# Kernel tuning notes

Measured on AMD Instinct MI355X. Metric: run time of the kernel, lower is better.

Reference implementation:

```python
import jax, jax.numpy as jnp
import numpy as np

N1, N2 = 262144, 65536          # dense / coarse point counts (packed batch)
PREV, SKIP, M0, M1 = 512, 256, 256, 256
EPS_BN = 1e-5                    # torch BatchNorm1d default eps
EPS_DIST = 1e-8


def _bn(x, g, b):
    # BatchNorm1d in training mode: biased batch stats over the point axis
    m = x.mean(axis=0)
    v = x.var(axis=0)
    return (x - m) * jax.lax.rsqrt(v + EPS_BN) * g + b


def setup_inputs() -> dict:
    key = jax.random.key(0)
    ks = jax.random.split(key, 8)
    inp = {
        "points1": jax.random.normal(ks[0], (N1, SKIP), jnp.float32),
        "points2": jax.random.normal(ks[1], (N2, PREV), jnp.float32),
        "dist": jax.random.uniform(ks[2], (N1, 3), jnp.float32),
        "idx": jax.random.randint(ks[3], (N1, 3), 0, N2, dtype=jnp.int32),
        # mlp_f0 / norm_f0
        "Wf0": jax.random.normal(ks[4], (PREV, M0), jnp.float32) / np.sqrt(PREV).astype(np.float32),
        "bf0": jnp.zeros((M0,), jnp.float32),
        "gf0": jnp.ones((M0,), jnp.float32),
        "betaf0": jnp.zeros((M0,), jnp.float32),
        # mlp_s0 / norm_s0 (skip path)
        "Ws0": jax.random.normal(ks[5], (SKIP, M0), jnp.float32) / np.sqrt(SKIP).astype(np.float32),
        "bs0": jnp.zeros((M0,), jnp.float32),
        "gs0": jnp.ones((M0,), jnp.float32),
        "betas0": jnp.zeros((M0,), jnp.float32),
        # mlp_convs[0] / mlp_bns[0]
        "W1": jax.random.normal(ks[6], (M0, M1), jnp.float32) / np.sqrt(M0).astype(np.float32),
        "b1": jnp.zeros((M1,), jnp.float32),
        "g1": jnp.ones((M1,), jnp.float32),
        "beta1": jnp.zeros((M1,), jnp.float32),
    }
    return inp


def reference(points1, points2, dist, idx, Wf0, bf0, gf0, betaf0,
              Ws0, bs0, gs0, betas0, W1, b1, g1, beta1):
    # f0 MLP + BN on coarse features: [N2, PREV] -> [N2, M0]
    p2 = _bn(points2 @ Wf0 + bf0, gf0, betaf0)
    # inverse-distance weights over 3 neighbors: [N1, 3]
    dr = 1.0 / (dist + EPS_DIST)
    w = dr / dr.sum(axis=1, keepdims=True)
    # fused gather + weighted sum: p2[idx] is [N1, 3, M0]
    interp = jnp.einsum('nkc,nk->nc', p2[idx], w)
    # skip path: [N1, SKIP] -> [N1, M0]
    skip = _bn(points1 @ Ws0 + bs0, gs0, betas0)
    x = jax.nn.relu(interp + skip)
    # mlp_convs stack (one layer here): Linear + BN + ReLU
    x = jax.nn.relu(_bn(x @ W1 + b1, g1, beta1))
    return x
```

## Files before the change

kernel.cpp:

```cpp
#include <hip/hip_runtime.h>
#include <hip/hip_bf16.h>

#define CN1 262144
#define CN2 65536
#define CPREV 512
#define CSKIP 256

using u16 = unsigned short;

typedef __attribute__((ext_vector_type(8))) short short8;
typedef __attribute__((ext_vector_type(8))) unsigned short ushort8;
typedef __attribute__((ext_vector_type(4))) float f32x4;
typedef __attribute__((ext_vector_type(8))) float f32x8;

__device__ __forceinline__ float toF(float v) { return v; }
__device__ __forceinline__ float toF(u16 u) { return __uint_as_float(((unsigned)u) << 16); }
__device__ __forceinline__ u16 f2bf(float f) {
    unsigned b = __float_as_uint(f);
    b += 0x7FFFu + ((b >> 16) & 1u);
    return (u16)(b >> 16);
}
__device__ __forceinline__ unsigned pack2(float lo, float hi) {
    return ((unsigned)f2bf(hi) << 16) | (unsigned)f2bf(lo);
}

__global__ __launch_bounds__(256) void transpose_all(
    const float* __restrict__ Wf0, const float* __restrict__ Ws0,
    const float* __restrict__ W1,
    u16* __restrict__ Wtf0, u16* __restrict__ Wts0, u16* __restrict__ Wt1)
{
    int b = blockIdx.x;
    const float* W; u16* Wt; int ksh, e;
    if (b < 512)      { W = Wf0; Wt = Wtf0; ksh = 9; e = b * 256 + threadIdx.x; }
    else if (b < 768) { W = Ws0; Wt = Wts0; ksh = 8; e = (b - 512) * 256 + threadIdx.x; }
    else              { W = W1;  Wt = Wt1;  ksh = 8; e = (b - 768) * 256 + threadIdx.x; }
    int K = 1 << ksh;
    int n = e >> ksh;
    int k = e & (K - 1);
    Wt[e] = f2bf(W[((size_t)k << 8) + n]);
}

template<typename OT>
__device__ __forceinline__ void epilogue(
    f32x4 (&acc)[4][4], u16* AsU, u16* BsU,
    const float* __restrict__ bias, OT* __restrict__ C,
    float* __restrict__ partial, int bm, int t)
{
    const int lane = t & 63;
    const int wid = t >> 6;
    const int wr = wid >> 1;
    const int wrow = wid >> 2;
    const int wcol = wid & 3;
    __syncthreads();
    float* cs  = (float*)AsU;
    float* cs2 = ((float*)AsU) + 512;
    const int r4 = (lane >> 4) * 4;
    const int cc = lane & 15;
    float bv[4];
#pragma unroll
    for (int ni = 0; ni < 4; ++ni) bv[ni] = bias[wcol * 64 + ni * 16 + cc];

#pragma unroll
    for (int ni = 0; ni < 4; ++ni) {
        int col = wcol * 64 + ni * 16 + cc;
        float s = 0.f, s2 = 0.f;
#pragma unroll
        for (int mi = 0; mi < 4; ++mi) {
#pragma unroll
            for (int j = 0; j < 4; ++j) {
                float val = acc[mi][ni][j] + bv[ni];
                s += val;
                s2 = fmaf(val, val, s2);
            }
        }
        s  += __shfl_xor(s, 16);  s  += __shfl_xor(s, 32);
        s2 += __shfl_xor(s2, 16); s2 += __shfl_xor(s2, 32);
        if (lane < 16) { cs[wrow * 256 + col] = s; cs2[wrow * 256 + col] = s2; }
    }

    if constexpr (sizeof(OT) == 2) {
        u16* patchw = BsU + wid * (16 * 72);
        const int trow = lane >> 2;
        const int c16 = (lane & 3) * 16;
#pragma unroll
        for (int mi = 0; mi < 4; ++mi) {
            __syncthreads();
#pragma unroll
            for (int ni = 0; ni < 4; ++ni)
#pragma unroll
                for (int j = 0; j < 4; ++j)
                    patchw[(r4 + j) * 72 + ni * 16 + cc] = f2bf(acc[mi][ni][j] + bv[ni]);
            __syncthreads();
            ushort8 u0 = *(const ushort8*)&patchw[trow * 72 + c16];
            ushort8 u1 = *(const ushort8*)&patchw[trow * 72 + c16 + 8];
            size_t r = (size_t)bm + wrow * 64 + mi * 16 + trow;
            size_t cb = (size_t)wcol * 64 + c16;
            *(ushort8*)((u16*)C + r * 256 + cb) = u0;
            *(ushort8*)((u16*)C + r * 256 + cb + 8) = u1;
        }
    } else {
        float* patchf = ((float*)BsU) + wid * (16 * 36);
        const int trow = lane >> 2;
        const int c8 = (lane & 3) * 8;
#pragma unroll
        for (int mi = 0; mi < 4; ++mi) {
#pragma unroll
            for (int np = 0; np < 2; ++np) {
                __syncthreads();
#pragma unroll
                for (int h = 0; h < 2; ++h) {
                    int ni = np * 2 + h;
#pragma unroll
                    for (int j = 0; j < 4; ++j)
                        patchf[(r4 + j) * 36 + h * 16 + cc] = acc[mi][ni][j] + bv[ni];
                }
                __syncthreads();
                float4 v0 = *(float4*)&patchf[trow * 36 + c8];
                float4 v1 = *(float4*)&patchf[trow * 36 + c8 + 4];
                size_t r = (size_t)bm + wrow * 64 + mi * 16 + trow;
                size_t cb = (size_t)wcol * 64 + np * 32 + c8;
                *(float4*)((float*)C + r * 256 + cb) = v0;
                *(float4*)((float*)C + r * 256 + cb + 4) = v1;
            }
        }
    }
    __syncthreads();
    if (t < 256) {
        partial[(size_t)blockIdx.x * 512 + t]       = cs[t] + cs[256 + t];
        partial[(size_t)blockIdx.x * 512 + 256 + t] = cs2[t] + cs2[256 + t];
    }
    (void)wr;
}

template<int K, typename OT>
__global__ __launch_bounds__(512) void gemm_mfma(
    const float* __restrict__ Af, const u16* __restrict__ Wt,
    const float* __restrict__ bias, OT* __restrict__ C,
    float* __restrict__ partial)
{
    __shared__ u16 As[128 * 40];
    __shared__ u16 Bs[256 * 40];
    const int t = threadIdx.x;
    const int bm = blockIdx.x * 128;
    const int lane = t & 63;
    const int wid = t >> 6;
    const int wrow = wid >> 2;
    const int wcol = wid & 3;

    const int arow = t >> 2;
    const int koff = (t & 3) * 8;

    f32x4 acc[4][4] = {};

    float4 ga0A, ga1A, ga0B, ga1B;
    ushort8 gb0A, gb1A, gb0B, gb1B;

    auto LOADA = [&](int k0) {
        const float* p = Af + (size_t)(bm + arow) * K + k0 + koff;
        ga0A = *(const float4*)p;
        ga1A = *(const float4*)(p + 4);
        const u16* q = Wt + (size_t)arow * K + k0 + koff;
        gb0A = *(const ushort8*)q;
        gb1A = *(const ushort8*)(q + (size_t)128 * K);
    };
    auto LOADB = [&](int k0) {
        const float* p = Af + (size_t)(bm + arow) * K + k0 + koff;
        ga0B = *(const float4*)p;
        ga1B = *(const float4*)(p + 4);
        const u16* q = Wt + (size_t)arow * K + k0 + koff;
        gb0B = *(const ushort8*)q;
        gb1B = *(const ushort8*)(q + (size_t)128 * K);
    };
    auto STAGE = [&](const float4& g0, const float4& g1,
                     const ushort8& b0, const ushort8& b1) {
        uint4 w;
        w.x = pack2(g0.x, g0.y);
        w.y = pack2(g0.z, g0.w);
        w.z = pack2(g1.x, g1.y);
        w.w = pack2(g1.z, g1.w);
        *(uint4*)&As[arow * 40 + koff] = w;
        *(ushort8*)&Bs[arow * 40 + koff] = b0;
        *(ushort8*)&Bs[(128 + arow) * 40 + koff] = b1;
    };
    auto MMA = [&]() {
        const int kq = (lane >> 4) * 8;
        const int rr = lane & 15;
        short8 af[4];
#pragma unroll
        for (int mi = 0; mi < 4; ++mi)
            af[mi] = *(const short8*)&As[(wrow * 64 + mi * 16 + rr) * 40 + kq];
#pragma unroll
        for (int ni = 0; ni < 4; ++ni) {
            short8 bf = *(const short8*)&Bs[(wcol * 64 + ni * 16 + rr) * 40 + kq];
#pragma unroll
            for (int mi = 0; mi < 4; ++mi)
                acc[mi][ni] = __builtin_amdgcn_mfma_f32_16x16x32_bf16(
                    af[mi], bf, acc[mi][ni], 0, 0, 0);
        }
    };

    constexpr int nk = K >> 5;
    LOADA(0);
    LOADB(32);
#pragma unroll
    for (int it = 0; it < nk; it += 2) {
        __syncthreads();
        STAGE(ga0A, ga1A, gb0A, gb1A);
        __syncthreads();
        if (it + 2 < nk) LOADA((it + 2) << 5);
        MMA();
        __syncthreads();
        STAGE(ga0B, ga1B, gb0B, gb1B);
        __syncthreads();
        if (it + 3 < nk) LOADB((it + 3) << 5);
        MMA();
    }

    epilogue<OT>(acc, As, Bs, bias, C, partial, bm, t);
}

template<typename OT>
__global__ __launch_bounds__(512) void gemm_fused(
    const u16* __restrict__ skipb, const u16* __restrict__ y2,
    const float* __restrict__ dist, const int* __restrict__ idx,
    const float* __restrict__ ssf, const float* __restrict__ sss,
    const u16* __restrict__ Wt, const float* __restrict__ bias,
    OT* __restrict__ C, float* __restrict__ partial)
{
    constexpr int K = 256;
    __shared__ u16 As[128 * 40];
    __shared__ u16 Bs[256 * 40];
    __shared__ float sstab[768];
    const int t = threadIdx.x;
    const int bm = blockIdx.x * 128;
    const int lane = t & 63;
    const int wid = t >> 6;
    const int wrow = wid >> 2;
    const int wcol = wid & 3;

    const int arow = t >> 2;
    const int koff = (t & 3) * 8;
    const int row = bm + arow;

    for (int e = t; e < 768; e += 512)
        sstab[e] = (e < 256) ? ssf[e] : sss[e - 256];

    float d0 = dist[row * 3 + 0], d1 = dist[row * 3 + 1], d2 = dist[row * 3 + 2];
    float r0 = 1.f / (d0 + 1e-8f), r1 = 1.f / (d1 + 1e-8f), r2 = 1.f / (d2 + 1e-8f);
    float inv = 1.f / (r0 + r1 + r2);
    const float w0 = r0 * inv, w1 = r1 * inv, w2 = r2 * inv;
    const size_t i0 = (size_t)idx[row * 3 + 0];
    const size_t i1 = (size_t)idx[row * 3 + 1];
    const size_t i2 = (size_t)idx[row * 3 + 2];

    f32x4 acc[4][4] = {};

    ushort8 skA, a0A, a1A, a2A, gb0A, gb1A;
    ushort8 skB, a0B, a1B, a2B, gb0B, gb1B;

    auto LOADA = [&](int k0) {
        const int kc = k0 + koff;
        skA = *(const ushort8*)(skipb + (size_t)row * 256 + kc);
        a0A = *(const ushort8*)(y2 + i0 * 256 + kc);
        a1A = *(const ushort8*)(y2 + i1 * 256 + kc);
        a2A = *(const ushort8*)(y2 + i2 * 256 + kc);
        const u16* q = Wt + (size_t)arow * K + kc;
        gb0A = *(const ushort8*)q;
        gb1A = *(const ushort8*)(q + (size_t)128 * K);
    };
    auto LOADB = [&](int k0) {
        const int kc = k0 + koff;
        skB = *(const ushort8*)(skipb + (size_t)row * 256 + kc);
        a0B = *(const ushort8*)(y2 + i0 * 256 + kc);
        a1B = *(const ushort8*)(y2 + i1 * 256 + kc);
        a2B = *(const ushort8*)(y2 + i2 * 256 + kc);
        const u16* q = Wt + (size_t)arow * K + kc;
        gb0B = *(const ushort8*)q;
        gb1B = *(const ushort8*)(q + (size_t)128 * K);
    };
    auto STAGE = [&](int it, const ushort8& sk8, const ushort8& a0,
                     const ushort8& a1, const ushort8& a2,
                     const ushort8& b0, const ushort8& b1) {
        const int kc = (it << 5) + koff;
        f32x8 sf = *(const f32x8*)&sstab[kc];
        f32x8 sx = *(const f32x8*)&sstab[256 + kc];
        f32x8 ch = *(const f32x8*)&sstab[512 + kc];
        float xs[8];
#pragma unroll
        for (int j = 0; j < 8; ++j) {
            float iv = w0 * toF((u16)a0[j]) + w1 * toF((u16)a1[j])
                     + w2 * toF((u16)a2[j]);
            float val = fmaf(iv, sf[j], fmaf(toF((u16)sk8[j]), sx[j], ch[j]));
            xs[j] = fmaxf(val, 0.f);
        }
        uint4 w;
        w.x = pack2(xs[0], xs[1]);
        w.y = pack2(xs[2], xs[3]);
        w.z = pack2(xs[4], xs[5]);
        w.w = pack2(xs[6], xs[7]);
        *(uint4*)&As[arow * 40 + koff] = w;
        *(ushort8*)&Bs[arow * 40 + koff] = b0;
        *(ushort8*)&Bs[(128 + arow) * 40 + koff] = b1;
    };
    auto MMA = [&]() {
        const int kq = (lane >> 4) * 8;
        const int rr = lane & 15;
        short8 af[4];
#pragma unroll
        for (int mi = 0; mi < 4; ++mi)
            af[mi] = *(const short8*)&As[(wrow * 64 + mi * 16 + rr) * 40 + kq];
#pragma unroll
        for (int ni = 0; ni < 4; ++ni) {
            short8 bf = *(const short8*)&Bs[(wcol * 64 + ni * 16 + rr) * 40 + kq];
#pragma unroll
            for (int mi = 0; mi < 4; ++mi)
                acc[mi][ni] = __builtin_amdgcn_mfma_f32_16x16x32_bf16(
                    af[mi], bf, acc[mi][ni], 0, 0, 0);
        }
    };

    constexpr int nk = K >> 5;
    LOADA(0);
    LOADB(32);
#pragma unroll
    for (int it = 0; it < nk; it += 2) {
        __syncthreads();
        STAGE(it, skA, a0A, a1A, a2A, gb0A, gb1A);
        __syncthreads();
        if (it + 2 < nk) LOADA((it + 2) << 5);
        MMA();
        __syncthreads();
        STAGE(it + 1, skB, a0B, a1B, a2B, gb0B, gb1B);
        __syncthreads();
        if (it + 3 < nk) LOADB((it + 3) << 5);
        MMA();
    }

    epilogue<OT>(acc, As, Bs, bias, C, partial, bm, t);
}

__global__ __launch_bounds__(256) void colstats_final_par(
    const float* __restrict__ partial, int nb, float invR,
    const float* __restrict__ g, const float* __restrict__ beta,
    const float* __restrict__ fold, float* __restrict__ ss)
{
    int c = blockIdx.x;
    int t = threadIdx.x;
    float s = 0.f, s2 = 0.f;
    for (int b = t; b < nb; b += 256) {
        s  += partial[(size_t)b * 512 + c];
        s2 += partial[(size_t)b * 512 + 256 + c];
    }
#pragma unroll
    for (int o = 32; o > 0; o >>= 1) {
        s += __shfl_xor(s, o);
        s2 += __shfl_xor(s2, o);
    }
    __shared__ float rs[4], rs2[4];
    if ((t & 63) == 0) { rs[t >> 6] = s; rs2[t >> 6] = s2; }
    __syncthreads();
    if (t == 0) {
        float S  = rs[0] + rs[1] + rs[2] + rs[3];
        float S2 = rs2[0] + rs2[1] + rs2[2] + rs2[3];
        float m = S * invR;
        float var = fmaf(-m, m, S2 * invR);
        float scale = g[c] * rsqrtf(var + 1e-5f);
        float shift = fmaf(-m, scale, beta[c]);
        if (fold) shift += fold[256 + c];
        ss[c] = scale;
        ss[256 + c] = shift;
    }
}

__global__ __launch_bounds__(256) void bn_relu_cvt(
    const u16* __restrict__ y3, float* __restrict__ out,
    const float* __restrict__ ss)
{
    size_t e = ((size_t)blockIdx.x * 256 + threadIdx.x) * 8;
    int kc = (int)(e & 255);
    ushort8 v = *(const ushort8*)(y3 + e);
    f32x8 sc = *(const f32x8*)(ss + kc);
    f32x8 sh = *(const f32x8*)(ss + 256 + kc);
    float4 o0, o1;
    o0.x = fmaxf(fmaf(toF((u16)v[0]), sc[0], sh[0]), 0.f);
    o0.y = fmaxf(fmaf(toF((u16)v[1]), sc[1], sh[1]), 0.f);
    o0.z = fmaxf(fmaf(toF((u16)v[2]), sc[2], sh[2]), 0.f);
    o0.w = fmaxf(fmaf(toF((u16)v[3]), sc[3], sh[3]), 0.f);
    o1.x = fmaxf(fmaf(toF((u16)v[4]), sc[4], sh[4]), 0.f);
    o1.y = fmaxf(fmaf(toF((u16)v[5]), sc[5], sh[5]), 0.f);
    o1.z = fmaxf(fmaf(toF((u16)v[6]), sc[6], sh[6]), 0.f);
    o1.w = fmaxf(fmaf(toF((u16)v[7]), sc[7], sh[7]), 0.f);
    *(float4*)(out + e) = o0;
    *(float4*)(out + e + 4) = o1;
}

__global__ __launch_bounds__(256) void bn_relu_inplace(
    float* __restrict__ out, const float* __restrict__ ss)
{
    size_t i4 = (size_t)blockIdx.x * 256 + threadIdx.x;
    int c4 = (int)(i4 & 63);
    float4 v = reinterpret_cast<float4*>(out)[i4];
    float4 sc = reinterpret_cast<const float4*>(ss)[c4];
    float4 sh = reinterpret_cast<const float4*>(ss + 256)[c4];
    v.x = fmaxf(fmaf(v.x, sc.x, sh.x), 0.f);
    v.y = fmaxf(fmaf(v.y, sc.y, sh.y), 0.f);
    v.z = fmaxf(fmaf(v.z, sc.z, sh.z), 0.f);
    v.w = fmaxf(fmaf(v.w, sc.w, sh.w), 0.f);
    reinterpret_cast<float4*>(out)[i4] = v;
}

extern "C" void kernel_launch(void* const* d_in, const int* in_sizes, int n_in,
                              void* d_out, int out_size, void* d_ws, size_t ws_size,
                              hipStream_t stream) {
    const float* points1 = (const float*)d_in[0];
    const float* points2 = (const float*)d_in[1];
    const float* dist    = (const float*)d_in[2];
    const int*   idx     = (const int*)d_in[3];
    const float* Wf0     = (const float*)d_in[4];
    const float* bf0     = (const float*)d_in[5];
    const float* gf0     = (const float*)d_in[6];
    const float* betaf0  = (const float*)d_in[7];
    const float* Ws0     = (const float*)d_in[8];
    const float* bs0     = (const float*)d_in[9];
    const float* gs0     = (const float*)d_in[10];
    const float* betas0  = (const float*)d_in[11];
    const float* W1      = (const float*)d_in[12];
    const float* b1      = (const float*)d_in[13];
    const float* g1      = (const float*)d_in[14];
    const float* beta1   = (const float*)d_in[15];

    u16* ws = (u16*)d_ws;
    size_t off = 0;
    u16* y2   = ws + off;  off += (size_t)CN2 * 256;
    u16* xbuf = ws + off;  off += (size_t)CN1 * 256;
    u16* Wtf0 = ws + off;  off += 512 * 256;
    u16* Wts0 = ws + off;  off += 256 * 256;
    u16* Wt1  = ws + off;  off += 256 * 256;
    float* partial = (float*)(ws + off); off += (size_t)2048 * 512 * 2;
    float* ss_f0 = (float*)(ws + off); off += 1024;
    float* ss_s0 = (float*)(ws + off); off += 1024;
    float* ss_1  = (float*)(ws + off); off += 1024;
    u16* y3 = ws + off;
    const size_t NEED = (off + (size_t)CN1 * 256) * 2;
    const bool fused_y3 = (ws_size >= NEED);
    float* out = (float*)d_out;

    transpose_all<<<1024, 256, 0, stream>>>(Wf0, Ws0, W1, Wtf0, Wts0, Wt1);

    gemm_mfma<512, u16><<<CN2 / 128, 512, 0, stream>>>(
        points2, Wtf0, bf0, y2, partial);
    colstats_final_par<<<256, 256, 0, stream>>>(partial, CN2 / 128, 1.0f / CN2,
                                                gf0, betaf0, nullptr, ss_f0);
    gemm_mfma<256, u16><<<CN1 / 128, 512, 0, stream>>>(
        points1, Wts0, bs0, xbuf, partial);
    colstats_final_par<<<256, 256, 0, stream>>>(partial, CN1 / 128, 1.0f / CN1,
                                                gs0, betas0, ss_f0, ss_s0);
    if (fused_y3) {
        gemm_fused<u16><<<CN1 / 128, 512, 0, stream>>>(
            xbuf, y2, dist, idx, ss_f0, ss_s0, Wt1, b1, y3, partial);
    } else {
        gemm_fused<float><<<CN1 / 128, 512, 0, stream>>>(
            xbuf, y2, dist, idx, ss_f0, ss_s0, Wt1, b1, out, partial);
    }
    colstats_final_par<<<256, 256, 0, stream>>>(partial, CN1 / 128, 1.0f / CN1,
                                                g1, beta1, nullptr, ss_1);
    if (fused_y3) {
        bn_relu_cvt<<<32768, 256, 0, stream>>>(y3, out, ss_1);
    } else {
        bn_relu_inplace<<<CN1 / 4, 256, 0, stream>>>(out, ss_1);
    }
}
```

Measured before the change: 409.2 us.

## Prebuild full fused A tile in LDS with warp-per-row coalesced gathers

New measurement: 428.8 us. +4.8%, slower.

```diff
diff --git a/kernel.cpp b/kernel.cpp
--- a/kernel.cpp
+++ b/kernel.cpp
@@ -41,19 +41,18 @@
 }
 
 template<typename OT>
-__device__ __forceinline__ void epilogue(
-    f32x4 (&acc)[4][4], u16* AsU, u16* BsU,
+__device__ __forceinline__ void epilogue8(
+    f32x4 (&acc)[4][4], u16* CsU, u16* PatchU,
     const float* __restrict__ bias, OT* __restrict__ C,
     float* __restrict__ partial, int bm, int t)
 {
     const int lane = t & 63;
     const int wid = t >> 6;
-    const int wr = wid >> 1;
     const int wrow = wid >> 2;
     const int wcol = wid & 3;
     __syncthreads();
-    float* cs  = (float*)AsU;
-    float* cs2 = ((float*)AsU) + 512;
+    float* cs  = (float*)CsU;
+    float* cs2 = ((float*)CsU) + 512;
     const int r4 = (lane >> 4) * 4;
     const int cc = lane & 15;
     float bv[4];
@@ -79,7 +78,7 @@
     }
 
     if constexpr (sizeof(OT) == 2) {
-        u16* patchw = BsU + wid * (16 * 72);
+        u16* patchw = PatchU + wid * 1152;
         const int trow = lane >> 2;
         const int c16 = (lane & 3) * 16;
 #pragma unroll
@@ -99,7 +98,7 @@
             *(ushort8*)((u16*)C + r * 256 + cb + 8) = u1;
         }
     } else {
-        float* patchf = ((float*)BsU) + wid * (16 * 36);
+        float* patchf = (float*)(PatchU + wid * 1152);
         const int trow = lane >> 2;
         const int c8 = (lane & 3) * 8;
 #pragma unroll
@@ -129,7 +128,6 @@
         partial[(size_t)blockIdx.x * 512 + t]       = cs[t] + cs[256 + t];
         partial[(size_t)blockIdx.x * 512 + 256 + t] = cs2[t] + cs2[256 + t];
     }
-    (void)wr;
 }
 
 template<int K, typename OT>
@@ -216,7 +214,7 @@
         MMA();
     }
 
-    epilogue<OT>(acc, As, Bs, bias, C, partial, bm, t);
+    epilogue8<OT>(acc, As, Bs, bias, C, partial, bm, t);
 }
 
 template<typename OT>
@@ -228,7 +226,7 @@
     OT* __restrict__ C, float* __restrict__ partial)
 {
     constexpr int K = 256;
-    __shared__ u16 As[128 * 40];
+    __shared__ u16 Ax[128 * 264];
     __shared__ u16 Bs[256 * 40];
     __shared__ float sstab[768];
     const int t = threadIdx.x;
@@ -238,77 +236,37 @@
     const int wrow = wid >> 2;
     const int wcol = wid & 3;
 
-    const int arow = t >> 2;
-    const int koff = (t & 3) * 8;
-    const int row = bm + arow;
+    const int brow = t >> 1;
+    const int bko = (t & 1) * 16;
+    const int rr = lane & 15;
+    const int kq = (lane >> 4) * 8;
 
     for (int e = t; e < 768; e += 512)
         sstab[e] = (e < 256) ? ssf[e] : sss[e - 256];
-
-    float d0 = dist[row * 3 + 0], d1 = dist[row * 3 + 1], d2 = dist[row * 3 + 2];
-    float r0 = 1.f / (d0 + 1e-8f), r1 = 1.f / (d1 + 1e-8f), r2 = 1.f / (d2 + 1e-8f);
-    float inv = 1.f / (r0 + r1 + r2);
-    const float w0 = r0 * inv, w1 = r1 * inv, w2 = r2 * inv;
-    const size_t i0 = (size_t)idx[row * 3 + 0];
-    const size_t i1 = (size_t)idx[row * 3 + 1];
-    const size_t i2 = (size_t)idx[row * 3 + 2];
+    __syncthreads();
+
+    const int col4 = lane * 4;
+    f32x4 sf = *(const f32x4*)&sstab[col4];
+    f32x4 sx = *(const f32x4*)&sstab[256 + col4];
+    f32x4 ch = *(const f32x4*)&sstab[512 + col4];
 
     f32x4 acc[4][4] = {};
-
-    ushort8 skA, a0A, a1A, a2A, gb0A, gb1A;
-    ushort8 skB, a0B, a1B, a2B, gb0B, gb1B;
-
-    auto LOADA = [&](int k0) {
-        const int kc = k0 + koff;
-        skA = *(const ushort8*)(skipb + (size_t)row * 256 + kc);
-        a0A = *(const ushort8*)(y2 + i0 * 256 + kc);
-        a1A = *(const ushort8*)(y2 + i1 * 256 + kc);
-        a2A = *(const ushort8*)(y2 + i2 * 256 + kc);
-        const u16* q = Wt + (size_t)arow * K + kc;
-        gb0A = *(const ushort8*)q;
-        gb1A = *(const ushort8*)(q + (size_t)128 * K);
-    };
+    ushort8 gb0, gb1;
+
     auto LOADB = [&](int k0) {
-        const int kc = k0 + koff;
-        skB = *(const ushort8*)(skipb + (size_t)row * 256 + kc);
-        a0B = *(const ushort8*)(y2 + i0 * 256 + kc);
-        a1B = *(const ushort8*)(y2 + i1 * 256 + kc);
-        a2B = *(const ushort8*)(y2 + i2 * 256 + kc);
-        const u16* q = Wt + (size_t)arow * K + kc;
-        gb0B = *(const ushort8*)q;
-        gb1B = *(const ushort8*)(q + (size_t)128 * K);
-    };
-    auto STAGE = [&](int it, const ushort8& sk8, const ushort8& a0,
-                     const ushort8& a1, const ushort8& a2,
-                     const ushort8& b0, const ushort8& b1) {
-        const int kc = (it << 5) + koff;
-        f32x8 sf = *(const f32x8*)&sstab[kc];
-        f32x8 sx = *(const f32x8*)&sstab[256 + kc];
-        f32x8 ch = *(const f32x8*)&sstab[512 + kc];
-        float xs[8];
-#pragma unroll
-        for (int j = 0; j < 8; ++j) {
-            float iv = w0 * toF((u16)a0[j]) + w1 * toF((u16)a1[j])
-                     + w2 * toF((u16)a2[j]);
-            float val = fmaf(iv, sf[j], fmaf(toF((u16)sk8[j]), sx[j], ch[j]));
-            xs[j] = fmaxf(val, 0.f);
-        }
-        uint4 w;
-        w.x = pack2(xs[0], xs[1]);
-        w.y = pack2(xs[2], xs[3]);
-        w.z = pack2(xs[4], xs[5]);
-        w.w = pack2(xs[6], xs[7]);
-        *(uint4*)&As[arow * 40 + koff] = w;
-        *(ushort8*)&Bs[arow * 40 + koff] = b0;
-        *(ushort8*)&Bs[(128 + arow) * 40 + koff] = b1;
-    };
-    auto MMA = [&]() {
-        const int kq = (lane >> 4) * 8;
-        const int rr = lane & 15;
+        const u16* q = Wt + (size_t)brow * K + k0 + bko;
+        gb0 = *(const ushort8*)q;
+        gb1 = *(const ushort8*)(q + 8);
+    };
+    auto STAGEB = [&]() {
+        *(ushort8*)&Bs[brow * 40 + bko] = gb0;
+        *(ushort8*)&Bs[brow * 40 + bko + 8] = gb1;
+    };
+    auto MMA = [&](int it) {
         short8 af[4];
 #pragma unroll
         for (int mi = 0; mi < 4; ++mi)
-            af[mi] = *(const short8*)&As[(wrow * 64 + mi * 16 + rr) * 40 + kq];
+            af[mi] = *(const short8*)&Ax[(wrow * 64 + mi * 16 + rr) * 264 + it * 32 + kq];
 #pragma unroll
         for (int ni = 0; ni < 4; ++ni) {
             short8 bf = *(const short8*)&Bs[(wcol * 64 + ni * 16 + rr) * 40 + kq];
@@ -319,24 +277,67 @@
         }
     };
 
-    constexpr int nk = K >> 5;
-    LOADA(0);
-    LOADB(32);
-#pragma unroll
-    for (int it = 0; it < nk; it += 2) {
-        __syncthreads();
-        STAGE(it, skA, a0A, a1A, a2A, gb0A, gb1A);
-        __syncthreads();
-        if (it + 2 < nk) LOADA((it + 2) << 5);
-        MMA();
-        __syncthreads();
-        STAGE(it + 1, skB, a0B, a1B, a2B, gb0B, gb1B);
-        __syncthreads();
-        if (it + 3 < nk) LOADB((it + 3) << 5);
-        MMA();
-    }
-
-    epilogue<OT>(acc, As, Bs, bias, C, partial, bm, t);
+#pragma unroll
+    for (int g = 0; g < 4; ++g) {
+        ushort4 sk[4], a0[4], a1[4], a2[4];
+        float w0[4], w1[4], w2[4];
+#pragma unroll
+        for (int u = 0; u < 4; ++u) {
+            const int r = wid * 16 + g * 4 + u;
+            const int row = bm + r;
+            float d0 = dist[row * 3 + 0], d1 = dist[row * 3 + 1], d2 = dist[row * 3 + 2];
+            float r0 = 1.f / (d0 + 1e-8f), r1 = 1.f / (d1 + 1e-8f), r2 = 1.f / (d2 + 1e-8f);
+            float inv = 1.f / (r0 + r1 + r2);
+            w0[u] = r0 * inv; w1[u] = r1 * inv; w2[u] = r2 * inv;
+            const size_t i0 = (size_t)(unsigned)idx[row * 3 + 0];
+            const size_t i1 = (size_t)(unsigned)idx[row * 3 + 1];
+            const size_t i2 = (size_t)(unsigned)idx[row * 3 + 2];
+            sk[u] = *(const ushort4*)(skipb + (size_t)row * 256 + col4);
+            a0[u] = *(const ushort4*)(y2 + i0 * 256 + col4);
+            a1[u] = *(const ushort4*)(y2 + i1 * 256 + col4);
+            a2[u] = *(const ushort4*)(y2 + i2 * 256 + col4);
+        }
+#pragma unroll
+        for (int u = 0; u < 4; ++u) {
+            const int r = wid * 16 + g * 4 + u;
+            float xs[4];
+            {
+                float iv = w0[u] * toF((u16)a0[u].x) + w1[u] * toF((u16)a1[u].x)
+                         + w2[u] * toF((u16)a2[u].x);
+                xs[0] = fmaxf(fmaf(iv, sf[0], fmaf(toF((u16)sk[u].x), sx[0], ch[0])), 0.f);
+            }
+            {
+                float iv = w0[u] * toF((u16)a0[u].y) + w1[u] * toF((u16)a1[u].y)
+                         + w2[u] * toF((u16)a2[u].y);
+                xs[1] = fmaxf(fmaf(iv, sf[1], fmaf(toF((u16)sk[u].y), sx[1], ch[1])), 0.f);
+            }
+            {
+                float iv = w0[u] * toF((u16)a0[u].z) + w1[u] * toF((u16)a1[u].z)
+                         + w2[u] * toF((u16)a2[u].z);
+                xs[2] = fmaxf(fmaf(iv, sf[2], fmaf(toF((u16)sk[u].z), sx[2], ch[2])), 0.f);
+            }
+            {
+                float iv = w0[u] * toF((u16)a0[u].w) + w1[u] * toF((u16)a1[u].w)
+                         + w2[u] * toF((u16)a2[u].w);
+                xs[3] = fmaxf(fmaf(iv, sf[3], fmaf(toF((u16)sk[u].w), sx[3], ch[3])), 0.f);
+            }
+            uint2 wv;
+            wv.x = pack2(xs[0], xs[1]);
+            wv.y = pack2(xs[2], xs[3]);
+            *(uint2*)&Ax[r * 264 + col4] = wv;
+        }
+    }
+
+    LOADB(0);
+    for (int it = 0; it < 8; ++it) {
+        __syncthreads();
+        STAGEB();
+        __syncthreads();
+        if (it + 1 < 8) LOADB((it + 1) * 32);
+        MMA(it);
+    }
+
+    epilogue8<OT>(acc, Ax, Bs, bias, C, partial, bm, t);
 }
 
 __global__ __launch_bounds__(256) void colstats_final_par(
```
